# Kernel tuning notes

Measured on AMD Instinct MI355X. Metric: run time of the kernel, lower is better.

## Reference

```python
import jax, jax.numpy as jnp
import numpy as np

B, S, D, H = 2, 2048, 1024, 16
DK = D // H


def setup_inputs() -> dict:
    key = jax.random.key(0)
    ks = jax.random.split(key, 11)
    scale = 1.0 / np.sqrt(D)
    inp = {
        "query": jax.random.normal(ks[0], (B, S, D), dtype=jnp.float32),
        "key": jax.random.normal(ks[1], (B, S, D), dtype=jnp.float32),
        "value": jax.random.normal(ks[2], (B, S, D), dtype=jnp.float32),
        "Wq": jax.random.normal(ks[3], (D, D), dtype=jnp.float32) * scale,
        "bq": jnp.zeros((D,), dtype=jnp.float32),
        "Wk": jax.random.normal(ks[4], (D, D), dtype=jnp.float32) * scale,
        "bk": jnp.zeros((D,), dtype=jnp.float32),
        "Wv": jax.random.normal(ks[5], (D, D), dtype=jnp.float32) * scale,
        "bv": jnp.zeros((D,), dtype=jnp.float32),
        "Wo": jax.random.normal(ks[6], (D, D), dtype=jnp.float32) * scale,
        "bo": jnp.zeros((D,), dtype=jnp.float32),
    }
    return inp


def _split_heads(x):
    # [B,S,D] -> [B,H,S,DK]
    b, s, _ = x.shape
    return x.reshape(b, s, H, DK).transpose(0, 2, 1, 3)


def reference(query, key, value, Wq, bq, Wk, bk, Wv, bv, Wo, bo):
    q = _split_heads(query @ Wq.T + bq)
    k = _split_heads(key @ Wk.T + bk)
    v = _split_heads(value @ Wv.T + bv)
    # scaled dot-product attention: [B,H,S,S]
    scores = jnp.einsum("bhqd,bhkd->bhqk", q, k) / np.sqrt(DK).astype(np.float32)
    attn = jax.nn.softmax(scores, axis=-1)  # stable max-subtract softmax, same math
    ctx = jnp.einsum("bhqk,bhkd->bhqd", attn, v)  # [B,H,S,DK]
    ctx = ctx.transpose(0, 2, 1, 3).reshape(query.shape[0], -1, H * DK)
    return ctx @ Wo.T + bo
```

## Files before the change

kernel.cpp:

```cpp
#include <hip/hip_runtime.h>
#include <math.h>

constexpr int NB = 2;
constexpr int NS = 2048;
constexpr int ND = 1024;
constexpr int NH = 16;
constexpr int NDK = 64;

typedef __attribute__((ext_vector_type(8))) short short8;
typedef __attribute__((ext_vector_type(4))) float floatx4;

__device__ inline unsigned short f2bf(float x) {
    unsigned u = __builtin_bit_cast(unsigned, x);
    u += 0x7fffu + ((u >> 16) & 1u);
    return (unsigned short)(u >> 16);
}

__device__ inline uint4 pack8(float4 a, float4 b) {
    unsigned short t[8] = {f2bf(a.x), f2bf(a.y), f2bf(a.z), f2bf(a.w),
                           f2bf(b.x), f2bf(b.y), f2bf(b.z), f2bf(b.w)};
    return *(uint4*)t;
}

#define GLOAD_LDS16(g, l) __builtin_amdgcn_global_load_lds( \
    (const __attribute__((address_space(1))) void*)(g),     \
    (__attribute__((address_space(3))) void*)(l), 16, 0, 0)

#define QSCALE 0.18033688f

__global__ __launch_bounds__(256) void cvt_all(
    const float* __restrict__ s0, const float* __restrict__ s1,
    const float* __restrict__ s2, const float* __restrict__ s3,
    const float* __restrict__ s4, const float* __restrict__ s5,
    const float* __restrict__ s6,
    unsigned short* __restrict__ d0, unsigned short* __restrict__ d1,
    unsigned short* __restrict__ d2, unsigned short* __restrict__ d3,
    unsigned short* __restrict__ d4, unsigned short* __restrict__ d5,
    unsigned short* __restrict__ d6)
{
    const int y = blockIdx.y;
    const float* srcs[7] = {s0, s1, s2, s3, s4, s5, s6};
    unsigned short* dsts[7] = {d0, d1, d2, d3, d4, d5, d6};
    const int nel = (y < 3) ? NB * NS * ND : ND * ND;
    int i = (blockIdx.x * 256 + threadIdx.x) * 8;
    if (i >= nel) return;
    const float* s = srcs[y];
    unsigned short* d = dsts[y];
    float4 a = *(const float4*)(s + i);
    float4 b = *(const float4*)(s + i + 4);
    *(uint4*)(d + i) = pack8(a, b);
}

template<int QA, int QB>
__device__ __forceinline__ void mfma_quad(
    floatx4 (&acc)[8][4], const short8 (&ta)[4][2], const short8 (&tb)[2][2][2])
{
#pragma unroll
    for (int ii = 0; ii < 4; ++ii)
#pragma unroll
        for (int jj = 0; jj < 2; ++jj) {
            acc[QA * 4 + ii][QB * 2 + jj] = __builtin_amdgcn_mfma_f32_16x16x32_bf16(
                ta[ii][0], tb[QB][jj][0], acc[QA * 4 + ii][QB * 2 + jj], 0, 0, 0);
            acc[QA * 4 + ii][QB * 2 + jj] = __builtin_amdgcn_mfma_f32_16x16x32_bf16(
                ta[ii][1], tb[QB][jj][1], acc[QA * 4 + ii][QB * 2 + jj], 0, 0, 0);
        }
}

__global__ __launch_bounds__(512, 2) void gemm_qkv(
    const unsigned short* __restrict__ Xq, const unsigned short* __restrict__ Xk,
    const unsigned short* __restrict__ Xv,
    const unsigned short* __restrict__ Wq, const unsigned short* __restrict__ Wk,
    const unsigned short* __restrict__ Wv,
    const float* __restrict__ bq, const float* __restrict__ bk,
    const float* __restrict__ bv,
    unsigned short* __restrict__ Cq, unsigned short* __restrict__ Ck,
    unsigned short* __restrict__ Cv)
{
    __shared__ unsigned short As[2][256 * 64];
    __shared__ unsigned short Bs[2][256 * 64];

    const int tid = threadIdx.x, w = tid >> 6, lane = tid & 63;
    const int lo = lane & 15, quad = lane >> 4;
    const int bid = blockIdx.x;
    const int seg = bid >> 6;
    const int idx = bid & 63;
    const int xcd = idx & 7;
    const int t8  = idx >> 3;
    const int K = ND;

    int bm, bn;
    const unsigned short *A, *Bw;
    const float* bias;
    if (seg == 2) {
        bm = t8 & 3; bn = (t8 >> 2) * 8 + xcd;
        A = Wv; Bw = Xv; bias = bv;
    } else {
        bn = t8 & 3; bm = (t8 >> 2) * 8 + xcd;
        if (seg == 1) { A = Xk; Bw = Wk; bias = bk; }
        else          { A = Xq; Bw = Wq; bias = bq; }
    }

    const int WM = (w >> 2) * 128, WN = (w & 3) * 64;

    const int srow = tid >> 3;
    const int sgo  = ((tid & 7) ^ (srow & 7)) * 8;
    const unsigned short* Asrc = A  + (size_t)(bm * 256 + srow) * K + sgo;
    const unsigned short* Bsrc = Bw + (size_t)(bn * 256 + srow) * K + sgo;

#define SA(bf_, t_, s_) GLOAD_LDS16(Asrc + (size_t)(s_) * 64 * K + (t_) * 64, \
                                    &As[bf_][(s_) * 4096 + tid * 8])
#define SB(bf_, t_, s_) GLOAD_LDS16(Bsrc + (size_t)(s_) * 64 * K + (t_) * 64, \
                                    &Bs[bf_][(s_) * 4096 + tid * 8])

    const int rp0 = ((quad) ^ (lo & 7)) * 8;
    const int rp1 = ((4 + quad) ^ (lo & 7)) * 8;

    short8 ta[4][2], tb[2][2][2];

#define RDA(bf_, qa_) { _Pragma("unroll") \
    for (int ii = 0; ii < 4; ++ii) { \
        const unsigned short* p_ = &As[bf_][(WM + (qa_) * 64 + ii * 16 + lo) * 64]; \
        ta[ii][0] = *(const short8*)(p_ + rp0); \
        ta[ii][1] = *(const short8*)(p_ + rp1); } }
#define RDB(bf_, qb_) { _Pragma("unroll") \
    for (int jj = 0; jj < 2; ++jj) { \
        const unsigned short* p_ = &Bs[bf_][(WN + (qb_) * 32 + jj * 16 + lo) * 64]; \
        tb[qb_][jj][0] = *(const short8*)(p_ + rp0); \
        tb[qb_][jj][1] = *(const short8*)(p_ + rp1); } }

#define PH_SYNC1 __builtin_amdgcn_s_barrier(); \
    asm volatile("s_waitcnt lgkmcnt(0)" ::: "memory"); \
    __builtin_amdgcn_sched_barrier(0); \
    __builtin_amdgcn_s_setprio(1);
#define PH_SYNC2 __builtin_amdgcn_s_setprio(0); \
    __builtin_amdgcn_sched_barrier(0); \
    __builtin_amdgcn_s_barrier();

    floatx4 acc[8][4];
#pragma unroll
    for (int i = 0; i < 8; ++i)
#pragma unroll
        for (int j = 0; j < 4; ++j) acc[i][j] = (floatx4){0.f, 0.f, 0.f, 0.f};

    SB(0, 0, 0); SB(0, 0, 1); SB(0, 0, 2); SB(0, 0, 3);
    SA(0, 0, 0); SA(0, 0, 1); SA(0, 0, 2); SA(0, 0, 3);
    SB(1, 1, 0); SB(1, 1, 1); SB(1, 1, 2); SB(1, 1, 3);
    asm volatile("s_waitcnt vmcnt(4)" ::: "memory");
    __builtin_amdgcn_s_barrier();

    constexpr int NIT = ND / 128;
#pragma unroll 1
    for (int it = 0; it < NIT; ++it) {
        const bool nl = (it < NIT - 1);
        const int t1 = 2 * it + 1, t2 = 2 * it + 2, t3 = 2 * it + 3;

        RDA(0, 0); RDB(0, 0);
        SA(1, t1, 0); SA(1, t1, 1);
        PH_SYNC1; mfma_quad<0, 0>(acc, ta, tb); PH_SYNC2;

        RDB(0, 1);
        SA(1, t1, 2); SA(1, t1, 3);
        PH_SYNC1; mfma_quad<0, 1>(acc, ta, tb); PH_SYNC2;

        RDA(0, 1);
        if (nl) { SB(0, t2, 0); SB(0, t2, 1); }
        PH_SYNC1; mfma_quad<1, 1>(acc, ta, tb); PH_SYNC2;

        if (nl) { SB(0, t2, 2); SB(0, t2, 3); }
        if (nl) asm volatile("s_waitcnt vmcnt(4)" ::: "memory");
        else    asm volatile("s_waitcnt vmcnt(0)" ::: "memory");
        PH_SYNC1; mfma_quad<1, 0>(acc, ta, tb); PH_SYNC2;

        RDA(1, 0); RDB(1, 0);
        if (nl) { SA(0, t2, 0); SA(0, t2, 1); }
        PH_SYNC1; mfma_quad<0, 0>(acc, ta, tb); PH_SYNC2;

        RDB(1, 1);
        if (nl) { SA(0, t2, 2); SA(0, t2, 3); }
        PH_SYNC1; mfma_quad<0, 1>(acc, ta, tb); PH_SYNC2;

        RDA(1, 1);
        if (nl) { SB(1, t3, 0); SB(1, t3, 1); }
        PH_SYNC1; mfma_quad<1, 1>(acc, ta, tb); PH_SYNC2;

        if (nl) { SB(1, t3, 2); SB(1, t3, 3); }
        if (nl) asm volatile("s_waitcnt vmcnt(4)" ::: "memory");
        PH_SYNC1; mfma_quad<1, 0>(acc, ta, tb); PH_SYNC2;
    }

#undef SA
#undef SB
#undef RDA
#undef RDB
#undef PH_SYNC1
#undef PH_SYNC2

    if (seg < 2) {
        unsigned short* C = seg ? Ck : Cq;
        const float scale = seg ? 1.f : QSCALE;
#pragma unroll
        for (int j = 0; j < 4; ++j) {
            const int col = bn * 256 + WN + j * 16 + lo;
            const float bb = bias[col];
#pragma unroll
            for (int i = 0; i < 8; ++i)
#pragma unroll
                for (int r = 0; r < 4; ++r) {
                    const int row = bm * 256 + WM + i * 16 + quad * 4 + r;
                    C[(size_t)row * ND + col] = f2bf((acc[i][j][r] + bb) * scale);
                }
        }
    } else {
#pragma unroll
        for (int i = 0; i < 8; ++i)
#pragma unroll
            for (int r = 0; r < 4; ++r) {
                const int row = bm * 256 + WM + i * 16 + quad * 4 + r;
                const float bb = bias[row];
#pragma unroll
                for (int j = 0; j < 4; ++j) {
                    const int col = bn * 256 + WN + j * 16 + lo;
                    const int b = col >> 11, s = col & (NS - 1);
                    Cv[(size_t)(b * ND + row) * NS + s] = f2bf(acc[i][j][r] + bb);
                }
            }
    }
}

constexpr int PRS = 72;

__global__ __launch_bounds__(256, 4) void attn_mfma(
    const unsigned short* __restrict__ qb,
    const unsigned short* __restrict__ kb,
    const unsigned short* __restrict__ vt,
    float* __restrict__ cacc0, float* __restrict__ cacc1,
    float* __restrict__ lbuf)
{
    __shared__ unsigned short Ks[64 * 64];
    __shared__ unsigned short Vs[64 * 64];
    __shared__ unsigned short Pt[4][32 * PRS];

    const int tid = threadIdx.x, w = tid >> 6, lane = tid & 63;
    const int lo = lane & 15, quad = lane >> 4;
    const int bid = blockIdx.x;
    const int xcd = bid & 7;
    const int tt  = bid >> 3;
    const int qgrp = tt & 15;
    const int bhk  = (tt >> 4) * 8 + xcd;
    const int bh = bhk >> 1, ksp = bhk & 1;
    const int b = bh >> 4, h = bh & 15;
    const int q0 = qgrp * 128 + w * 32;

    short8 qf[2][2];
    #pragma unroll
    for (int qt = 0; qt < 2; ++qt) {
        const unsigned short* qrow =
            qb + (size_t)(b * NS + q0 + qt * 16 + lo) * ND + h * NDK + quad * 8;
        qf[qt][0] = *(const short8*)(qrow);
        qf[qt][1] = *(const short8*)(qrow + 32);
    }

    const int c0 = tid, c1 = tid + 256;
    const int r0 = c0 >> 3, g0 = (c0 & 7) ^ (r0 & 7);
    const int r1 = c1 >> 3, g1 = (c1 & 7) ^ (r1 & 7);
    const unsigned short* Ksrc0 = kb + (size_t)(b * NS + r0) * ND + h * NDK + g0 * 8;
    const unsigned short* Ksrc1 = kb + (size_t)(b * NS + r1) * ND + h * NDK + g1 * 8;
    const unsigned short* Vsrc0 = vt + (size_t)(bh * NDK + r0) * NS + g0 * 8;
    const unsigned short* Vsrc1 = vt + (size_t)(bh * NDK + r1) * NS + g1 * 8;
    unsigned short* Kd0 = Ks + c0 * 8;
    unsigned short* Kd1 = Ks + c1 * 8;
    unsigned short* Vd0 = Vs + c0 * 8;
    unsigned short* Vd1 = Vs + c1 * 8;

    floatx4 acc[2][4], lacc[2];
    #pragma unroll
    for (int qt = 0; qt < 2; ++qt) {
        lacc[qt] = (floatx4){0.f, 0.f, 0.f, 0.f};
        #pragma unroll
        for (int cb = 0; cb < 4; ++cb) acc[qt][cb] = (floatx4){0.f, 0.f, 0.f, 0.f};
    }

    const short8 ones = {0x3F80, 0x3F80, 0x3F80, 0x3F80,
                         0x3F80, 0x3F80, 0x3F80, 0x3F80};
    unsigned short* pw = &Pt[w][0];
    const int pos0 = (quad ^ (lo & 7)) * 8;
    const int pos1 = ((4 + quad) ^ (lo & 7)) * 8;

    for (int key0 = ksp * 1024; key0 < ksp * 1024 + 1024; key0 += 64) {
        GLOAD_LDS16(Ksrc0 + (size_t)key0 * ND, Kd0);
        GLOAD_LDS16(Ksrc1 + (size_t)key0 * ND, Kd1);
        GLOAD_LDS16(Vsrc0 + key0, Vd0);
        GLOAD_LDS16(Vsrc1 + key0, Vd1);
        __syncthreads();

        floatx4 s[2][4];
        #pragma unroll
        for (int t = 0; t < 4; ++t) {
            const int rw = (t * 16 + lo) * 64;
            const short8 kf0 = *(const short8*)(Ks + rw + pos0);
            const short8 kf1 = *(const short8*)(Ks + rw + pos1);
            #pragma unroll
            for (int qt = 0; qt < 2; ++qt) {
                s[qt][t] = __builtin_amdgcn_mfma_f32_16x16x32_bf16(
                    kf0, qf[qt][0], (floatx4){0.f, 0.f, 0.f, 0.f}, 0, 0, 0);
                s[qt][t] = __builtin_amdgcn_mfma_f32_16x16x32_bf16(
                    kf1, qf[qt][1], s[qt][t], 0, 0, 0);
            }
        }

        #pragma unroll
        for (int qt = 0; qt < 2; ++qt)
            #pragma unroll
            for (int t = 0; t < 4; ++t) {
                unsigned u0 = __builtin_bit_cast(unsigned, __builtin_amdgcn_exp2f(s[qt][t][0]));
                unsigned u1 = __builtin_bit_cast(unsigned, __builtin_amdgcn_exp2f(s[qt][t][1]));
                unsigned u2 = __builtin_bit_cast(unsigned, __builtin_amdgcn_exp2f(s[qt][t][2]));
                unsigned u3 = __builtin_bit_cast(unsigned, __builtin_amdgcn_exp2f(s[qt][t][3]));
                uint2 pk = {(u0 >> 16) | (u1 & 0xFFFF0000u),
                            (u2 >> 16) | (u3 & 0xFFFF0000u)};
                *(uint2*)(pw + (qt * 16 + lo) * PRS + t * 16 + quad * 4) = pk;
            }

        short8 pf[2][2];
        #pragma unroll
        for (int qt = 0; qt < 2; ++qt) {
            pf[qt][0] = *(const short8*)(pw + (qt * 16 + lo) * PRS + quad * 8);
            pf[qt][1] = *(const short8*)(pw + (qt * 16 + lo) * PRS + 32 + quad * 8);
            lacc[qt] = __builtin_amdgcn_mfma_f32_16x16x32_bf16(pf[qt][0], ones, lacc[qt], 0, 0, 0);
            lacc[qt] = __builtin_amdgcn_mfma_f32_16x16x32_bf16(pf[qt][1], ones, lacc[qt], 0, 0, 0);
        }

        #pragma unroll
        for (int cb = 0; cb < 4; ++cb) {
            const int rw = (cb * 16 + lo) * 64;
            const short8 vf0 = *(const short8*)(Vs + rw + pos0);
            const short8 vf1 = *(const short8*)(Vs + rw + pos1);
            #pragma unroll
            for (int qt = 0; qt < 2; ++qt) {
                acc[qt][cb] = __builtin_amdgcn_mfma_f32_16x16x32_bf16(pf[qt][0], vf0, acc[qt][cb], 0, 0, 0);
                acc[qt][cb] = __builtin_amdgcn_mfma_f32_16x16x32_bf16(pf[qt][1], vf1, acc[qt][cb], 0, 0, 0);
            }
        }
        __syncthreads();
    }

    float* ca = ksp ? cacc1 : cacc0;
    float* lb = lbuf + (size_t)ksp * (NB * NH * NS);
    #pragma unroll
    for (int qt = 0; qt < 2; ++qt) {
        #pragma unroll
        for (int cb = 0; cb < 4; ++cb)
            #pragma unroll
            for (int r = 0; r < 4; ++r) {
                size_t off = (size_t)(b * NS + q0 + qt * 16 + quad * 4 + r) * ND
                           + h * NDK + cb * 16 + lo;
                ca[off] = acc[qt][cb][r];
            }
        if (lo == 0)
            #pragma unroll
            for (int r = 0; r < 4; ++r)
                lb[(size_t)bh * NS + q0 + qt * 16 + quad * 4 + r] = lacc[qt][r];
    }
}

__global__ __launch_bounds__(256) void gemm_o(
    const float* __restrict__ cacc0, const float* __restrict__ cacc1,
    const float* __restrict__ lbuf, const unsigned short* __restrict__ Bw,
    const float* __restrict__ bias, float* __restrict__ Cout)
{
    __shared__ unsigned short As[64 * 64];
    __shared__ unsigned short Bs[128 * 64];
    const int tid = threadIdx.x, w = tid >> 6, lane = tid & 63;
    const int lo = lane & 15, quad = lane >> 4;
    const int bid = blockIdx.x;
    const int xcd = bid & 7;
    const int tt  = bid >> 3;
    const int bn  = tt & 7;
    const int bm  = (tt >> 3) * 8 + xcd;
    const int K = ND;
    const int wm = (w >> 1) * 32, wn = (w & 1) * 64;
    const size_t LHALF = (size_t)NB * NH * NS;

    const int ar = tid >> 3;
    const int ag = (tid & 7) ^ (ar & 7);
    const int tok0 = bm * 64 + ar, tok1 = tok0 + 32;
    const float* A00 = cacc0 + (size_t)tok0 * ND + ag * 8;
    const float* A01 = cacc1 + (size_t)tok0 * ND + ag * 8;
    const float* A10 = cacc0 + (size_t)tok1 * ND + ag * 8;
    const float* A11 = cacc1 + (size_t)tok1 * ND + ag * 8;
    const size_t lb0 = (size_t)((tok0 >> 11) << 4) * NS + (tok0 & (NS - 1));
    const size_t lb1 = (size_t)((tok1 >> 11) << 4) * NS + (tok1 & (NS - 1));
    unsigned short* AsD0 = As + tid * 8;
    unsigned short* AsD1 = As + (tid + 256) * 8;

    const unsigned short* Bg[4];
    unsigned short* BsD[4];
    #pragma unroll
    for (int p = 0; p < 4; ++p) {
        int c = tid + 256 * p, r = c >> 3, g = (c & 7) ^ (r & 7);
        Bg[p] = Bw + (size_t)(bn * 128 + r) * K + g * 8;
        BsD[p] = Bs + c * 8;
    }

    floatx4 acc[2][4];
    #pragma unroll
    for (int i = 0; i < 2; ++i)
        #pragma unroll
        for (int j = 0; j < 4; ++j) acc[i][j] = (floatx4){0.f, 0.f, 0.f, 0.f};

    float4 ra[8];
    float lv0, lv1;
    ra[0] = *(const float4*)(A00);     ra[1] = *(const float4*)(A00 + 4);
    ra[2] = *(const float4*)(A01);     ra[3] = *(const float4*)(A01 + 4);
    ra[4] = *(const float4*)(A10);     ra[5] = *(const float4*)(A10 + 4);
    ra[6] = *(const float4*)(A11);     ra[7] = *(const float4*)(A11 + 4);
    lv0 = lbuf[lb0] + lbuf[lb0 + LHALF];
    lv1 = lbuf[lb1] + lbuf[lb1 + LHALF];

    for (int k0 = 0; k0 < K; k0 += 64) {
        const float inv0 = __builtin_amdgcn_rcpf(lv0);
        const float inv1 = __builtin_amdgcn_rcpf(lv1);
        __syncthreads();
        #pragma unroll
        for (int p = 0; p < 4; ++p) GLOAD_LDS16(Bg[p] + k0, BsD[p]);
        {
            float4 s0 = {(ra[0].x + ra[2].x) * inv0, (ra[0].y + ra[2].y) * inv0,
                         (ra[0].z + ra[2].z) * inv0, (ra[0].w + ra[2].w) * inv0};
            float4 s1 = {(ra[1].x + ra[3].x) * inv0, (ra[1].y + ra[3].y) * inv0,
                         (ra[1].z + ra[3].z) * inv0, (ra[1].w + ra[3].w) * inv0};
            *(uint4*)AsD0 = pack8(s0, s1);
            float4 s2 = {(ra[4].x + ra[6].x) * inv1, (ra[4].y + ra[6].y) * inv1,
                         (ra[4].z + ra[6].z) * inv1, (ra[4].w + ra[6].w) * inv1};
            float4 s3 = {(ra[5].x + ra[7].x) * inv1, (ra[5].y + ra[7].y) * inv1,
                         (ra[5].z + ra[7].z) * inv1, (ra[5].w + ra[7].w) * inv1};
            *(uint4*)AsD1 = pack8(s2, s3);
        }
        __syncthreads();

        const int kn = k0 + 64;
        if (kn < K) {
            ra[0] = *(const float4*)(A00 + kn); ra[1] = *(const float4*)(A00 + kn + 4);
            ra[2] = *(const float4*)(A01 + kn); ra[3] = *(const float4*)(A01 + kn + 4);
            ra[4] = *(const float4*)(A10 + kn); ra[5] = *(const float4*)(A10 + kn + 4);
            ra[6] = *(const float4*)(A11 + kn); ra[7] = *(const float4*)(A11 + kn + 4);
            const size_t hoff = (size_t)(kn >> 6) * NS;
            lv0 = lbuf[lb0 + hoff] + lbuf[lb0 + hoff + LHALF];
            lv1 = lbuf[lb1 + hoff] + lbuf[lb1 + hoff + LHALF];
        }

        #pragma unroll
        for (int s = 0; s < 2; ++s) {
            const int pos = ((s * 4 + quad) ^ (lo & 7)) * 8;
            short8 af[2], bf[4];
            #pragma unroll
            for (int i = 0; i < 2; ++i)
                af[i] = *(const short8*)(As + (wm + i * 16 + lo) * 64 + pos);
            #pragma unroll
            for (int j = 0; j < 4; ++j)
                bf[j] = *(const short8*)(Bs + (wn + j * 16 + lo) * 64 + pos);
            #pragma unroll
            for (int i = 0; i < 2; ++i)
                #pragma unroll
                for (int j = 0; j < 4; ++j)
                    acc[i][j] = __builtin_amdgcn_mfma_f32_16x16x32_bf16(af[i], bf[j], acc[i][j], 0, 0, 0);
        }
    }

    #pragma unroll
    for (int j = 0; j < 4; ++j) {
        const int col = bn * 128 + wn + j * 16 + lo;
        const float bb = bias[col];
        #pragma unroll
        for (int i = 0; i < 2; ++i)
            #pragma unroll
            for (int r = 0; r < 4; ++r) {
                const int row = bm * 64 + wm + i * 16 + quad * 4 + r;
                Cout[(size_t)row * ND + col] = acc[i][j][r] + bb;
            }
    }
}

extern "C" void kernel_launch(void* const* d_in, const int* in_sizes, int n_in,
                              void* d_out, int out_size, void* d_ws, size_t ws_size,
                              hipStream_t stream)
{
    const float* query = (const float*)d_in[0];
    const float* key   = (const float*)d_in[1];
    const float* value = (const float*)d_in[2];
    const float* Wq    = (const float*)d_in[3];
    const float* bq    = (const float*)d_in[4];
    const float* Wk    = (const float*)d_in[5];
    const float* bk    = (const float*)d_in[6];
    const float* Wv    = (const float*)d_in[7];
    const float* bv    = (const float*)d_in[8];
    const float* Wo    = (const float*)d_in[9];
    const float* bo    = (const float*)d_in[10];
    float* out = (float*)d_out;

    const size_t n  = (size_t)NB * NS * ND;
    const size_t nw = (size_t)ND * ND;

    unsigned short* X0   = (unsigned short*)d_ws;
    unsigned short* X1   = X0 + n;
    unsigned short* X2   = X1 + n;
    unsigned short* W0   = X2 + n;
    unsigned short* W1   = W0 + nw;
    unsigned short* W2   = W1 + nw;
    unsigned short* W3   = W2 + nw;
    unsigned short* qbuf = W3 + nw;
    unsigned short* kbuf = qbuf + n;
    unsigned short* vtb  = kbuf + n;
    float* cacc1 = (float*)(vtb + n);
    float* lbuf  = cacc1 + n;
    float* cacc0 = (float*)X1;

    cvt_all<<<dim3((int)(n / 2048), 7), 256, 0, stream>>>(
        query, key, value, Wq, Wk, Wv, Wo, X0, X1, X2, W0, W1, W2, W3);

    gemm_qkv<<<192, 512, 0, stream>>>(X0, X1, X2, W0, W1, W2,
                                      bq, bk, bv, qbuf, kbuf, vtb);

    attn_mfma<<<1024, 256, 0, stream>>>(qbuf, kbuf, vtb, cacc0, cacc1, lbuf);

    gemm_o<<<512, 256, 0, stream>>>(cacc0, cacc1, lbuf, W3, bo, out);
}
```

Measured before the change: 222.0 us.

## Double-buffer K/V tiles in attention with 512-thread blocks and prefetch

The attention kernel now uses 8 waves per block covering 256 query rows, so each K/V tile staged in LDS is reused by twice as many waves, and the grid is halved to 512 blocks. K/V tiles are double-buffered: the next tile's global-to-LDS load is issued before computing on the current one, with explicit vmcnt waits and raw s_barrier in place of __syncthreads. It also raises wave priority around the MFMA sections. The cost is more LDS per block, which may lower occupancy, plus reliance on hand-written waitcnt correctness.

```diff
diff --git a/kernel.cpp b/kernel.cpp
--- a/kernel.cpp
+++ b/kernel.cpp
@@ -229,27 +229,27 @@
 
 constexpr int PRS = 72;
 
-__global__ __launch_bounds__(256, 4) void attn_mfma(
+__global__ __launch_bounds__(512, 4) void attn_mfma(
     const unsigned short* __restrict__ qb,
     const unsigned short* __restrict__ kb,
     const unsigned short* __restrict__ vt,
     float* __restrict__ cacc0, float* __restrict__ cacc1,
     float* __restrict__ lbuf)
 {
-    __shared__ unsigned short Ks[64 * 64];
-    __shared__ unsigned short Vs[64 * 64];
-    __shared__ unsigned short Pt[4][32 * PRS];
+    __shared__ unsigned short Ks[2][64 * 64];
+    __shared__ unsigned short Vs[2][64 * 64];
+    __shared__ unsigned short Pt[8][32 * PRS];
 
     const int tid = threadIdx.x, w = tid >> 6, lane = tid & 63;
     const int lo = lane & 15, quad = lane >> 4;
     const int bid = blockIdx.x;
     const int xcd = bid & 7;
     const int tt  = bid >> 3;
-    const int qgrp = tt & 15;
-    const int bhk  = (tt >> 4) * 8 + xcd;
+    const int qgrp = tt & 7;
+    const int bhk  = (tt >> 3) * 8 + xcd;
     const int bh = bhk >> 1, ksp = bhk & 1;
     const int b = bh >> 4, h = bh & 15;
-    const int q0 = qgrp * 128 + w * 32;
+    const int q0 = qgrp * 256 + w * 32;
 
     short8 qf[2][2];
     #pragma unroll
@@ -260,17 +260,13 @@
         qf[qt][1] = *(const short8*)(qrow + 32);
     }
 
-    const int c0 = tid, c1 = tid + 256;
-    const int r0 = c0 >> 3, g0 = (c0 & 7) ^ (r0 & 7);
-    const int r1 = c1 >> 3, g1 = (c1 & 7) ^ (r1 & 7);
-    const unsigned short* Ksrc0 = kb + (size_t)(b * NS + r0) * ND + h * NDK + g0 * 8;
-    const unsigned short* Ksrc1 = kb + (size_t)(b * NS + r1) * ND + h * NDK + g1 * 8;
-    const unsigned short* Vsrc0 = vt + (size_t)(bh * NDK + r0) * NS + g0 * 8;
-    const unsigned short* Vsrc1 = vt + (size_t)(bh * NDK + r1) * NS + g1 * 8;
-    unsigned short* Kd0 = Ks + c0 * 8;
-    unsigned short* Kd1 = Ks + c1 * 8;
-    unsigned short* Vd0 = Vs + c0 * 8;
-    unsigned short* Vd1 = Vs + c1 * 8;
+    const int r0 = tid >> 3, g0 = (tid & 7) ^ (r0 & 7);
+    const unsigned short* Ksrc = kb + (size_t)(b * NS + r0) * ND + h * NDK + g0 * 8;
+    const unsigned short* Vsrc = vt + (size_t)(bh * NDK + r0) * NS + g0 * 8;
+
+#define STAGE(bf_, k_) { \
+    GLOAD_LDS16(Ksrc + (size_t)(k_) * ND, &Ks[bf_][tid * 8]); \
+    GLOAD_LDS16(Vsrc + (k_),              &Vs[bf_][tid * 8]); }
 
     floatx4 acc[2][4], lacc[2];
     #pragma unroll
@@ -286,19 +282,31 @@
     const int pos0 = (quad ^ (lo & 7)) * 8;
     const int pos1 = ((4 + quad) ^ (lo & 7)) * 8;
 
-    for (int key0 = ksp * 1024; key0 < ksp * 1024 + 1024; key0 += 64) {
-        GLOAD_LDS16(Ksrc0 + (size_t)key0 * ND, Kd0);
-        GLOAD_LDS16(Ksrc1 + (size_t)key0 * ND, Kd1);
-        GLOAD_LDS16(Vsrc0 + key0, Vd0);
-        GLOAD_LDS16(Vsrc1 + key0, Vd1);
-        __syncthreads();
+    const int kbase = ksp * 1024;
+    STAGE(0, kbase);
+
+    #pragma unroll 2
+    for (int it = 0; it < 16; ++it) {
+        const int bf = it & 1;
+        if (it < 15) {
+            STAGE(bf ^ 1, kbase + (it + 1) * 64);
+            asm volatile("s_waitcnt vmcnt(2)" ::: "memory");
+        } else {
+            asm volatile("s_waitcnt vmcnt(0)" ::: "memory");
+        }
+        __builtin_amdgcn_s_barrier();
+        __builtin_amdgcn_sched_barrier(0);
+
+        const unsigned short* Kc = Ks[bf];
+        const unsigned short* Vc = Vs[bf];
 
         floatx4 s[2][4];
+        __builtin_amdgcn_s_setprio(1);
         #pragma unroll
         for (int t = 0; t < 4; ++t) {
             const int rw = (t * 16 + lo) * 64;
-            const short8 kf0 = *(const short8*)(Ks + rw + pos0);
-            const short8 kf1 = *(const short8*)(Ks + rw + pos1);
+            const short8 kf0 = *(const short8*)(Kc + rw + pos0);
+            const short8 kf1 = *(const short8*)(Kc + rw + pos1);
             #pragma unroll
             for (int qt = 0; qt < 2; ++qt) {
                 s[qt][t] = __builtin_amdgcn_mfma_f32_16x16x32_bf16(
@@ -307,6 +315,7 @@
                     kf1, qf[qt][1], s[qt][t], 0, 0, 0);
             }
         }
+        __builtin_amdgcn_s_setprio(0);
 
         #pragma unroll
         for (int qt = 0; qt < 2; ++qt)
@@ -330,19 +339,24 @@
             lacc[qt] = __builtin_amdgcn_mfma_f32_16x16x32_bf16(pf[qt][1], ones, lacc[qt], 0, 0, 0);
         }
 
+        __builtin_amdgcn_s_setprio(1);
         #pragma unroll
         for (int cb = 0; cb < 4; ++cb) {
             const int rw = (cb * 16 + lo) * 64;
-            const short8 vf0 = *(const short8*)(Vs + rw + pos0);
-            const short8 vf1 = *(const short8*)(Vs + rw + pos1);
+            const short8 vf0 = *(const short8*)(Vc + rw + pos0);
+            const short8 vf1 = *(const short8*)(Vc + rw + pos1);
             #pragma unroll
             for (int qt = 0; qt < 2; ++qt) {
                 acc[qt][cb] = __builtin_amdgcn_mfma_f32_16x16x32_bf16(pf[qt][0], vf0, acc[qt][cb], 0, 0, 0);
                 acc[qt][cb] = __builtin_amdgcn_mfma_f32_16x16x32_bf16(pf[qt][1], vf1, acc[qt][cb], 0, 0, 0);
             }
         }
-        __syncthreads();
-    }
+        __builtin_amdgcn_s_setprio(0);
+
+        __builtin_amdgcn_sched_barrier(0);
+        __builtin_amdgcn_s_barrier();
+    }
+#undef STAGE
 
     float* ca = ksp ? cacc1 : cacc0;
     float* lb = lbuf + (size_t)ksp * (NB * NH * NS);
@@ -520,7 +534,7 @@
     gemm_qkv<<<192, 512, 0, stream>>>(X0, X1, X2, W0, W1, W2,
                                       bq, bk, bv, qbuf, kbuf, vtb);
 
-    attn_mfma<<<1024, 256, 0, stream>>>(qbuf, kbuf, vtb, cacc0, cacc1, lbuf);
+    attn_mfma<<<512, 512, 0, stream>>>(qbuf, kbuf, vtb, cacc0, cacc1, lbuf);
 
     gemm_o<<<512, 256, 0, stream>>>(cacc0, cacc1, lbuf, W3, bo, out);
 }
```

Measured after the change: 220.0 us. No clear change (-0.9%).
